# Optimization experiments

Measured on AMD Instinct MI355X. Metric: run time of the kernel, lower is better.

## Reference

```python
import jax, jax.numpy as jnp
import numpy as np

D_MODEL = 2048
D_FFN = 8192
RANK = 16
MOD_SCALE = 0.1
EPS = 1e-6


def setup_inputs() -> dict:
    key = jax.random.key(0)
    ks = jax.random.split(key, 8)
    B, S = 2, 2048
    init_scale = 0.01
    return {
        'hidden_states': jax.random.normal(ks[0], (B, S, D_MODEL), jnp.float32),
        'attn_output': jax.random.normal(ks[1], (B, S, D_MODEL), jnp.float32),
        'A': jax.random.normal(ks[2], (D_MODEL, RANK), jnp.float32) * (init_scale / np.sqrt(D_MODEL)),
        'Bmat': jax.random.normal(ks[3], (RANK, D_FFN), jnp.float32) * (init_scale / np.sqrt(RANK)),
        'W_in': jax.random.normal(ks[4], (D_FFN, D_MODEL), jnp.float32) * 0.02,  # gate_proj.weight
        'W_up': jax.random.normal(ks[5], (D_FFN, D_MODEL), jnp.float32) * 0.02,  # up_proj.weight
        'W_down': jax.random.normal(ks[6], (D_MODEL, D_FFN), jnp.float32) * 0.02,  # down_proj.weight
        'gamma': jnp.ones((D_MODEL,), jnp.float32),  # post_attention_layernorm (RMSNorm) weight
    }


def _rmsnorm(x, gamma):
    var = jnp.mean(x * x, axis=-1, keepdims=True)
    return x * jax.lax.rsqrt(var + EPS) * gamma


def reference(hidden_states, attn_output, A, Bmat, W_in, W_up, W_down, gamma):
    residual = hidden_states
    # Neuro-plastic modulation: [B,S,r]
    modulation = MOD_SCALE * jnp.tanh(jnp.einsum('bsd,dr->bsr', attn_output, A))
    # NPT applies post-attn norm to the residual (not residual+attn)
    h = _rmsnorm(residual, gamma)  # [B,S,d_model]
    # Fused per-token weight delta: delta_w^T @ h == B^T ((A^T h) * mod)
    hA = jnp.einsum('bsd,dr->bsr', h, A)  # [B,S,r]
    delta_out = jnp.einsum('bsr,rf->bsf', hA * modulation, Bmat)  # [B,S,d_ffn]
    gate = jax.nn.silu(jnp.einsum('bsd,fd->bsf', h, W_in) + delta_out)
    up = jnp.einsum('bsd,fd->bsf', h, W_up)
    out = jnp.einsum('bsf,df->bsd', gate * up, W_down)
    return residual + out
```

## Files before the change

kernel.cpp:

```cpp
#include <hip/hip_runtime.h>
#include <cstdint>
#include <cstddef>

#define D_MODEL 2048
#define D_FFN   8192
#define RANK    16
#define EPS     1e-6f
#define MOD_SCALE 0.1f

typedef float    f32x4 __attribute__((ext_vector_type(4)));
typedef _Float16 half8 __attribute__((ext_vector_type(8)));

__device__ __forceinline__ void async_load16(const void* g, void* l) {
  __builtin_amdgcn_global_load_lds(
      (const __attribute__((address_space(1))) uint32_t*)g,
      (__attribute__((address_space(3))) uint32_t*)l,
      16, 0, 0);
}

__device__ __forceinline__ void stage_tile(const _Float16* __restrict__ gbase,
                                           size_t stride, _Float16* lds, int tid) {
  #pragma unroll
  for (int j = 0; j < 4; ++j) {
    int idx = j * 256 + tid;
    int row = idx >> 3;
    int c   = (idx & 7) ^ (row & 7);
    async_load16(gbase + (size_t)row * stride + c * 8, &lds[idx * 8]);
  }
}

__device__ __forceinline__ half8 frag_read(const _Float16* lds, int r, int c) {
  return *(const half8*)&lds[r * 64 + ((c ^ (r & 7)) * 8)];
}

__global__ __launch_bounds__(256) void convert3_f32_f16(
    const float* __restrict__ s0, const float* __restrict__ s1,
    const float* __restrict__ s2,
    _Float16* __restrict__ d0, _Float16* __restrict__ d1,
    _Float16* __restrict__ d2)
{
  const int w = blockIdx.x >> 13;
  const float*   s = (w == 0) ? s0 : (w == 1) ? s1 : s2;
  _Float16*      d = (w == 0) ? d0 : (w == 1) ? d1 : d2;
  size_t i = ((size_t)(blockIdx.x & 8191) * 256 + threadIdx.x) * 8;
  f32x4 a = *(const f32x4*)(s + i);
  f32x4 b = *(const f32x4*)(s + i + 4);
  half8 h;
  #pragma unroll
  for (int j = 0; j < 4; ++j) { h[j] = (_Float16)a[j]; h[4+j] = (_Float16)b[j]; }
  *(half8*)(d + i) = h;
}

__global__ __launch_bounds__(256) void convert_f32_f16(
    const float* __restrict__ s, _Float16* __restrict__ d)
{
  size_t i = ((size_t)blockIdx.x * 256 + threadIdx.x) * 8;
  f32x4 a = *(const f32x4*)(s + i);
  f32x4 b = *(const f32x4*)(s + i + 4);
  half8 h;
  #pragma unroll
  for (int j = 0; j < 4; ++j) { h[j] = (_Float16)a[j]; h[4+j] = (_Float16)b[j]; }
  *(half8*)(d + i) = h;
}

__global__ __launch_bounds__(256) void prep_kernel(
    const float* __restrict__ hs, const float* __restrict__ attn,
    const float* __restrict__ Amat, const float* __restrict__ gamma,
    _Float16* __restrict__ h16, float* __restrict__ cmat)
{
  const int token = blockIdx.x;
  const int tid   = threadIdx.x;
  const int lane  = tid & 63;
  const int wv    = tid >> 6;
  const size_t tb = (size_t)token * D_MODEL;
  const int base  = tid * 8;

  f32x4 x0 = *(const f32x4*)(hs + tb + base);
  f32x4 x1 = *(const f32x4*)(hs + tb + base + 4);
  f32x4 a0 = *(const f32x4*)(attn + tb + base);
  f32x4 a1 = *(const f32x4*)(attn + tb + base + 4);

  float ss = 0.f;
  #pragma unroll
  for (int j = 0; j < 4; ++j) ss += x0[j]*x0[j] + x1[j]*x1[j];
  #pragma unroll
  for (int off = 32; off > 0; off >>= 1) ss += __shfl_xor(ss, off, 64);

  __shared__ float red[4];
  __shared__ float redp[4][RANK];
  __shared__ float redh[4][RANK];
  if (lane == 0) red[wv] = ss;
  __syncthreads();
  const float tot = red[0] + red[1] + red[2] + red[3];
  const float rms = rsqrtf(tot * (1.0f / D_MODEL) + EPS);

  f32x4 g0 = *(const f32x4*)(gamma + base);
  f32x4 g1 = *(const f32x4*)(gamma + base + 4);
  float hv[8], av[8];
  #pragma unroll
  for (int j = 0; j < 4; ++j) {
    hv[j]   = x0[j] * rms * g0[j];
    hv[4+j] = x1[j] * rms * g1[j];
    av[j]   = a0[j];
    av[4+j] = a1[j];
  }
  half8 hh;
  #pragma unroll
  for (int j = 0; j < 8; ++j) hh[j] = (_Float16)hv[j];
  *(half8*)(h16 + tb + base) = hh;

  float pa[RANK], ph[RANK];
  #pragma unroll
  for (int r = 0; r < RANK; ++r) { pa[r] = 0.f; ph[r] = 0.f; }
  #pragma unroll
  for (int e = 0; e < 8; ++e) {
    const f32x4* Ar = (const f32x4*)(Amat + (size_t)(base + e) * RANK);
    #pragma unroll
    for (int q = 0; q < 4; ++q) {
      f32x4 ar = Ar[q];
      #pragma unroll
      for (int j = 0; j < 4; ++j) {
        pa[q*4+j] += av[e] * ar[j];
        ph[q*4+j] += hv[e] * ar[j];
      }
    }
  }
  #pragma unroll
  for (int r = 0; r < RANK; ++r) {
    #pragma unroll
    for (int off = 32; off > 0; off >>= 1) {
      pa[r] += __shfl_xor(pa[r], off, 64);
      ph[r] += __shfl_xor(ph[r], off, 64);
    }
  }
  if (lane == 0) {
    #pragma unroll
    for (int r = 0; r < RANK; ++r) { redp[wv][r] = pa[r]; redh[wv][r] = ph[r]; }
  }
  __syncthreads();
  if (tid < RANK) {
    float sp = redp[0][tid] + redp[1][tid] + redp[2][tid] + redp[3][tid];
    float sh = redh[0][tid] + redh[1][tid] + redh[2][tid] + redh[3][tid];
    cmat[(size_t)token * RANK + tid] = sh * (MOD_SCALE * tanhf(sp));
  }
}

__global__ __launch_bounds__(256, 2) void gemm_gateup(
    const _Float16* __restrict__ h16,
    const _Float16* __restrict__ Wg16, const _Float16* __restrict__ Wu16,
    const float* __restrict__ cmat, const float* __restrict__ Bmat,
    _Float16* __restrict__ tmat)
{
  __shared__ __align__(16) _Float16 sA [128*64];
  __shared__ __align__(16) _Float16 sB1[128*64];
  __shared__ __align__(16) _Float16 sB2[128*64];

  const int tid  = threadIdx.x;
  const int lane = tid & 63;
  const int wv   = tid >> 6;
  const int wm   = (wv >> 1) * 64;
  const int wn   = (wv & 1) * 64;
  const int lr   = lane & 15;
  const int quad = lane >> 4;
  const int gm0  = blockIdx.y * 128;
  const int gn0  = blockIdx.x * 128;

  f32x4 accG[4][4], accU[4][4];
  #pragma unroll
  for (int i = 0; i < 4; ++i)
    #pragma unroll
    for (int j = 0; j < 4; ++j) {
      f32x4 z = {0.f, 0.f, 0.f, 0.f};
      accG[i][j] = z; accU[i][j] = z;
    }

  for (int kt = 0; kt < D_MODEL / 64; ++kt) {
    __syncthreads();
    stage_tile(h16  + (size_t)gm0 * D_MODEL + kt * 64, D_MODEL, sA,  tid);
    stage_tile(Wg16 + (size_t)gn0 * D_MODEL + kt * 64, D_MODEL, sB1, tid);
    stage_tile(Wu16 + (size_t)gn0 * D_MODEL + kt * 64, D_MODEL, sB2, tid);
    __syncthreads();
    #pragma unroll
    for (int ks = 0; ks < 2; ++ks) {
      const int ck = ks * 4 + quad;
      half8 af[4], bg[4], bu[4];
      #pragma unroll
      for (int im = 0; im < 4; ++im)
        af[im] = frag_read(sA, wm + im * 16 + lr, ck);
      #pragma unroll
      for (int in = 0; in < 4; ++in) {
        bg[in] = frag_read(sB1, wn + in * 16 + lr, ck);
        bu[in] = frag_read(sB2, wn + in * 16 + lr, ck);
      }
      #pragma unroll
      for (int im = 0; im < 4; ++im)
        #pragma unroll
        for (int in = 0; in < 4; ++in) {
          accG[im][in] = __builtin_amdgcn_mfma_f32_16x16x32_f16(af[im], bg[in], accG[im][in], 0, 0, 0);
          accU[im][in] = __builtin_amdgcn_mfma_f32_16x16x32_f16(af[im], bu[in], accU[im][in], 0, 0, 0);
        }
    }
  }

  __syncthreads();
  #pragma unroll
  for (int i = 0; i < 16; ++i) {
    int idx = i * 256 + tid;
    int m = idx >> 5, kk = idx & 31;
    sA[idx]  = (kk < RANK) ? (_Float16)cmat[(size_t)(gm0 + m) * RANK + kk] : (_Float16)0.0f;
    sB1[idx] = (kk < RANK) ? (_Float16)Bmat[(size_t)kk * D_FFN + gn0 + m]  : (_Float16)0.0f;
  }
  __syncthreads();
  {
    const int ko = quad * 8;
    half8 af[4], bd[4];
    #pragma unroll
    for (int im = 0; im < 4; ++im)
      af[im] = *(const half8*)&sA[(wm + im * 16 + lr) * 32 + ko];
    #pragma unroll
    for (int in = 0; in < 4; ++in)
      bd[in] = *(const half8*)&sB1[(wn + in * 16 + lr) * 32 + ko];
    #pragma unroll
    for (int im = 0; im < 4; ++im)
      #pragma unroll
      for (int in = 0; in < 4; ++in)
        accG[im][in] = __builtin_amdgcn_mfma_f32_16x16x32_f16(af[im], bd[in], accG[im][in], 0, 0, 0);
  }

  #pragma unroll
  for (int im = 0; im < 4; ++im)
    #pragma unroll
    for (int in = 0; in < 4; ++in) {
      const int growb = gm0 + wm + im * 16 + quad * 4;
      const int gcol  = gn0 + wn + in * 16 + lr;
      #pragma unroll
      for (int r = 0; r < 4; ++r) {
        float g = accG[im][in][r];
        float u = accU[im][in][r];
        float s = g / (1.0f + __expf(-g));
        tmat[(size_t)(growb + r) * D_FFN + gcol] = (_Float16)(s * u);
      }
    }
}

__global__ __launch_bounds__(256, 3) void gemm_down(
    const _Float16* __restrict__ tmat, const _Float16* __restrict__ Wd16,
    const float* __restrict__ hs, float* __restrict__ out)
{
  __shared__ __align__(16) _Float16 sA[128*64];
  __shared__ __align__(16) _Float16 sB[128*64];

  const int tid  = threadIdx.x;
  const int lane = tid & 63;
  const int wv   = tid >> 6;
  const int wm   = (wv >> 1) * 64;
  const int wn   = (wv & 1) * 64;
  const int lr   = lane & 15;
  const int quad = lane >> 4;
  const int gm0  = blockIdx.y * 128;
  const int gn0  = blockIdx.x * 128;

  f32x4 acc[4][4];
  #pragma unroll
  for (int i = 0; i < 4; ++i)
    #pragma unroll
    for (int j = 0; j < 4; ++j) {
      f32x4 z = {0.f, 0.f, 0.f, 0.f};
      acc[i][j] = z;
    }

  for (int kt = 0; kt < D_FFN / 64; ++kt) {
    __syncthreads();
    stage_tile(tmat + (size_t)gm0 * D_FFN + kt * 64, D_FFN, sA, tid);
    stage_tile(Wd16 + (size_t)gn0 * D_FFN + kt * 64, D_FFN, sB, tid);
    __syncthreads();
    #pragma unroll
    for (int ks = 0; ks < 2; ++ks) {
      const int ck = ks * 4 + quad;
      half8 af[4], bf_[4];
      #pragma unroll
      for (int im = 0; im < 4; ++im)
        af[im] = frag_read(sA, wm + im * 16 + lr, ck);
      #pragma unroll
      for (int in = 0; in < 4; ++in)
        bf_[in] = frag_read(sB, wn + in * 16 + lr, ck);
      #pragma unroll
      for (int im = 0; im < 4; ++im)
        #pragma unroll
        for (int in = 0; in < 4; ++in)
          acc[im][in] = __builtin_amdgcn_mfma_f32_16x16x32_f16(af[im], bf_[in], acc[im][in], 0, 0, 0);
    }
  }

  #pragma unroll
  for (int im = 0; im < 4; ++im)
    #pragma unroll
    for (int in = 0; in < 4; ++in) {
      const int growb = gm0 + wm + im * 16 + quad * 4;
      const int gcol  = gn0 + wn + in * 16 + lr;
      #pragma unroll
      for (int r = 0; r < 4; ++r) {
        size_t o = (size_t)(growb + r) * D_MODEL + gcol;
        out[o] = hs[o] + acc[im][in][r];
      }
    }
}

extern "C" void kernel_launch(void* const* d_in, const int* in_sizes, int n_in,
                              void* d_out, int out_size, void* d_ws, size_t ws_size,
                              hipStream_t stream) {
  const float* hs    = (const float*)d_in[0];
  const float* attn  = (const float*)d_in[1];
  const float* Amat  = (const float*)d_in[2];
  const float* Bmat  = (const float*)d_in[3];
  const float* Wg    = (const float*)d_in[4];
  const float* Wu    = (const float*)d_in[5];
  const float* Wd    = (const float*)d_in[6];
  const float* gamma = (const float*)d_in[7];
  float* out = (float*)d_out;

  const int M = in_sizes[0] / D_MODEL;
  const size_t WD = (size_t)D_FFN * D_MODEL;

  char* ws = (char*)d_ws;
  _Float16* h16  = (_Float16*)ws;
  float*    cmat = (float*)(ws + (size_t)M * D_MODEL * 2);
  _Float16* tmat = (_Float16*)(ws + (size_t)M * D_MODEL * 2 + (size_t)M * RANK * 4);
  _Float16* wbuf = tmat + (size_t)M * D_FFN;
  _Float16* Wg16 = wbuf;
  _Float16* Wu16 = wbuf + WD;

  const size_t base_bytes = (size_t)M * D_MODEL * 2 + (size_t)M * RANK * 4
                          + (size_t)M * D_FFN * 2 + 2 * WD * 2;
  const bool sep_wd = (ws_size >= base_bytes + WD * 2);
  _Float16* Wd16 = sep_wd ? (wbuf + 2 * WD) : wbuf;

  const int convBlocks = (int)(WD / (256 * 8));

  prep_kernel<<<M, 256, 0, stream>>>(hs, attn, Amat, gamma, h16, cmat);
  if (sep_wd) {
    convert3_f32_f16<<<3 * convBlocks, 256, 0, stream>>>(Wg, Wu, Wd, Wg16, Wu16, Wd16);
    gemm_gateup<<<dim3(D_FFN / 128, M / 128), 256, 0, stream>>>(h16, Wg16, Wu16, cmat, Bmat, tmat);
  } else {
    convert_f32_f16<<<convBlocks, 256, 0, stream>>>(Wg, Wg16);
    convert_f32_f16<<<convBlocks, 256, 0, stream>>>(Wu, Wu16);
    gemm_gateup<<<dim3(D_FFN / 128, M / 128), 256, 0, stream>>>(h16, Wg16, Wu16, cmat, Bmat, tmat);
    convert_f32_f16<<<convBlocks, 256, 0, stream>>>(Wd, Wd16);
  }
  gemm_down<<<dim3(D_MODEL / 128, M / 128), 256, 0, stream>>>(tmat, Wd16, hs, out);
}
```

Before: 769.3 us.

## Split-K the down projection GEMM into two halves with a reduction kernel

The down-projection GEMM grid (16x32 = 512 blocks) gets a second z-dimension that splits the K=8192 reduction into two halves. Half 0 writes residual plus its partial sum to out, half 1 writes its partial to a scratch buffer that reuses the Wu16 workspace, and a new reduce_add kernel sums them. This doubles block-level parallelism to fill the GPU better. The cost is an extra 16 MB fp32 write and read plus one more launch. In the fallback path the gate and up weight conversions are also merged into a single launch.

```diff
diff --git a/kernel.cpp b/kernel.cpp
--- a/kernel.cpp
+++ b/kernel.cpp
@@ -33,6 +33,22 @@
   return *(const half8*)&lds[r * 64 + ((c ^ (r & 7)) * 8)];
 }
 
+__global__ __launch_bounds__(256) void convert2_f32_f16(
+    const float* __restrict__ s0, const float* __restrict__ s1,
+    _Float16* __restrict__ d0, _Float16* __restrict__ d1)
+{
+  const int w = blockIdx.x >> 13;
+  const float* s = (w == 0) ? s0 : s1;
+  _Float16*    d = (w == 0) ? d0 : d1;
+  size_t i = ((size_t)(blockIdx.x & 8191) * 256 + threadIdx.x) * 8;
+  f32x4 a = *(const f32x4*)(s + i);
+  f32x4 b = *(const f32x4*)(s + i + 4);
+  half8 h;
+  #pragma unroll
+  for (int j = 0; j < 4; ++j) { h[j] = (_Float16)a[j]; h[4+j] = (_Float16)b[j]; }
+  *(half8*)(d + i) = h;
+}
+
 __global__ __launch_bounds__(256) void convert3_f32_f16(
     const float* __restrict__ s0, const float* __restrict__ s1,
     const float* __restrict__ s2,
@@ -40,8 +56,8 @@
     _Float16* __restrict__ d2)
 {
   const int w = blockIdx.x >> 13;
-  const float*   s = (w == 0) ? s0 : (w == 1) ? s1 : s2;
-  _Float16*      d = (w == 0) ? d0 : (w == 1) ? d1 : d2;
+  const float* s = (w == 0) ? s0 : (w == 1) ? s1 : s2;
+  _Float16*    d = (w == 0) ? d0 : (w == 1) ? d1 : d2;
   size_t i = ((size_t)(blockIdx.x & 8191) * 256 + threadIdx.x) * 8;
   f32x4 a = *(const f32x4*)(s + i);
   f32x4 b = *(const f32x4*)(s + i + 4);
@@ -61,6 +77,18 @@
   #pragma unroll
   for (int j = 0; j < 4; ++j) { h[j] = (_Float16)a[j]; h[4+j] = (_Float16)b[j]; }
   *(half8*)(d + i) = h;
+}
+
+__global__ __launch_bounds__(256) void reduce_add(
+    float* __restrict__ out, const float* __restrict__ part)
+{
+  size_t i = ((size_t)blockIdx.x * 256 + threadIdx.x) * 8;
+  f32x4 a0 = *(const f32x4*)(out + i);
+  f32x4 a1 = *(const f32x4*)(out + i + 4);
+  f32x4 b0 = *(const f32x4*)(part + i);
+  f32x4 b1 = *(const f32x4*)(part + i + 4);
+  *(f32x4*)(out + i)     = a0 + b0;
+  *(f32x4*)(out + i + 4) = a1 + b1;
 }
 
 __global__ __launch_bounds__(256) void prep_kernel(
@@ -245,7 +273,8 @@
 
 __global__ __launch_bounds__(256, 3) void gemm_down(
     const _Float16* __restrict__ tmat, const _Float16* __restrict__ Wd16,
-    const float* __restrict__ hs, float* __restrict__ out)
+    const float* __restrict__ hs, float* __restrict__ out,
+    float* __restrict__ part)
 {
   __shared__ __align__(16) _Float16 sA[128*64];
   __shared__ __align__(16) _Float16 sB[128*64];
@@ -259,6 +288,8 @@
   const int quad = lane >> 4;
   const int gm0  = blockIdx.y * 128;
   const int gn0  = blockIdx.x * 128;
+  const int kz   = blockIdx.z;
+  const int kbase = kz * (D_FFN / 2 / 64);
 
   f32x4 acc[4][4];
   #pragma unroll
@@ -269,10 +300,10 @@
       acc[i][j] = z;
     }
 
-  for (int kt = 0; kt < D_FFN / 64; ++kt) {
+  for (int kt = 0; kt < D_FFN / 2 / 64; ++kt) {
     __syncthreads();
-    stage_tile(tmat + (size_t)gm0 * D_FFN + kt * 64, D_FFN, sA, tid);
-    stage_tile(Wd16 + (size_t)gn0 * D_FFN + kt * 64, D_FFN, sB, tid);
+    stage_tile(tmat + (size_t)gm0 * D_FFN + (kbase + kt) * 64, D_FFN, sA, tid);
+    stage_tile(Wd16 + (size_t)gn0 * D_FFN + (kbase + kt) * 64, D_FFN, sB, tid);
     __syncthreads();
     #pragma unroll
     for (int ks = 0; ks < 2; ++ks) {
@@ -301,7 +332,8 @@
       #pragma unroll
       for (int r = 0; r < 4; ++r) {
         size_t o = (size_t)(growb + r) * D_MODEL + gcol;
-        out[o] = hs[o] + acc[im][in][r];
+        if (kz == 0) out[o]  = hs[o] + acc[im][in][r];
+        else         part[o] = acc[im][in][r];
       }
     }
 }
@@ -329,6 +361,7 @@
   _Float16* wbuf = tmat + (size_t)M * D_FFN;
   _Float16* Wg16 = wbuf;
   _Float16* Wu16 = wbuf + WD;
+  float*    part = (float*)Wu16;
 
   const size_t base_bytes = (size_t)M * D_MODEL * 2 + (size_t)M * RANK * 4
                           + (size_t)M * D_FFN * 2 + 2 * WD * 2;
@@ -342,10 +375,10 @@
     convert3_f32_f16<<<3 * convBlocks, 256, 0, stream>>>(Wg, Wu, Wd, Wg16, Wu16, Wd16);
     gemm_gateup<<<dim3(D_FFN / 128, M / 128), 256, 0, stream>>>(h16, Wg16, Wu16, cmat, Bmat, tmat);
   } else {
-    convert_f32_f16<<<convBlocks, 256, 0, stream>>>(Wg, Wg16);
-    convert_f32_f16<<<convBlocks, 256, 0, stream>>>(Wu, Wu16);
+    convert2_f32_f16<<<2 * convBlocks, 256, 0, stream>>>(Wg, Wu, Wg16, Wu16);
     gemm_gateup<<<dim3(D_FFN / 128, M / 128), 256, 0, stream>>>(h16, Wg16, Wu16, cmat, Bmat, tmat);
     convert_f32_f16<<<convBlocks, 256, 0, stream>>>(Wd, Wd16);
   }
-  gemm_down<<<dim3(D_MODEL / 128, M / 128), 256, 0, stream>>>(tmat, Wd16, hs, out);
-}
+  gemm_down<<<dim3(D_MODEL / 128, M / 128, 2), 256, 0, stream>>>(tmat, Wd16, hs, out, part);
+  reduce_add<<<(int)((size_t)M * D_MODEL / (256 * 8)), 256, 0, stream>>>(out, part);
+}
```

New measurement: 781.5 us. About the same (+1.6%).
